# Optimization experiments

Hardware: AMD Instinct MI355X
Metric: run time of the kernel (lower is better)

Reference implementation:

```python
import jax, jax.numpy as jnp
from jax import lax
import numpy as np
import math

D_MODEL = 1024
D_STATE = 16
D_CONV = 4
EXPAND = 2
D_INNER = EXPAND * D_MODEL  # 2048
DT_RANK = math.ceil(D_MODEL / 16)  # 64
BATCH = 2
SEQ = 2048


def setup_inputs() -> dict:
    key = jax.random.key(0)
    ks = jax.random.split(key, 8)
    s = 0.02
    x = jax.random.normal(ks[0], (BATCH, SEQ, D_MODEL), jnp.float32)
    ln_w = jnp.ones((D_MODEL,), jnp.float32)
    ln_b = jnp.zeros((D_MODEL,), jnp.float32)
    in_proj_w = jax.random.normal(ks[1], (D_MODEL, 2 * D_INNER), jnp.float32) * s
    conv_w = jax.random.normal(ks[2], (D_INNER, D_CONV), jnp.float32) * s
    conv_b = jnp.zeros((D_INNER,), jnp.float32)
    x_proj_w = jax.random.normal(ks[3], (D_INNER, DT_RANK + 2 * D_STATE), jnp.float32) * s
    dt_proj_w = jax.random.normal(ks[4], (DT_RANK, D_INNER), jnp.float32) * (DT_RANK ** -0.5)
    # mamba-ssm dt bias init: softplus^{-1}(dt) with dt ~ logUniform(1e-3, 1e-1)
    dt = jnp.exp(jax.random.uniform(ks[5], (D_INNER,), jnp.float32)
                 * (jnp.log(0.1) - jnp.log(0.001)) + jnp.log(0.001))
    dt_proj_b = dt + jnp.log(-jnp.expm1(-dt))
    # S4D-real init: A = -[1..d_state] per channel
    A_log = jnp.log(jnp.broadcast_to(
        jnp.arange(1, D_STATE + 1, dtype=jnp.float32), (D_INNER, D_STATE)))
    D_skip = jnp.ones((D_INNER,), jnp.float32)
    out_proj_w = jax.random.normal(ks[6], (D_INNER, D_MODEL), jnp.float32) * s
    return dict(x=x, ln_w=ln_w, ln_b=ln_b, in_proj_w=in_proj_w, conv_w=conv_w,
                conv_b=conv_b, x_proj_w=x_proj_w, dt_proj_w=dt_proj_w,
                dt_proj_b=dt_proj_b, A_log=A_log, D_skip=D_skip,
                out_proj_w=out_proj_w)


def _layernorm(x, w, b):
    mu = x.mean(-1, keepdims=True)
    var = ((x - mu) ** 2).mean(-1, keepdims=True)
    return (x - mu) * lax.rsqrt(var + 1e-5) * w + b


def _mamba(xn, in_proj_w, conv_w, conv_b, x_proj_w, dt_proj_w, dt_proj_b,
           A_log, D_skip, out_proj_w):
    # in_proj -> split into conv path and gate z
    xz = xn @ in_proj_w                      # [B, L, 2*d_inner]
    xi, z = jnp.split(xz, 2, axis=-1)
    # causal depthwise conv1d over time
    xc = jnp.pad(xi.transpose(0, 2, 1), ((0, 0), (0, 0), (D_CONV - 1, 0)))
    xc = lax.conv_general_dilated(xc, conv_w[:, None, :], (1,), 'VALID',
                                  feature_group_count=D_INNER,
                                  dimension_numbers=('NCH', 'OIH', 'NCH'))
    xc = jax.nn.silu(xc.transpose(0, 2, 1) + conv_b)   # [B, L, d_inner]
    # input-dependent dt, B, C
    dbc = xc @ x_proj_w                      # [B, L, dt_rank + 2*d_state]
    dt = jax.nn.softplus(dbc[..., :DT_RANK] @ dt_proj_w + dt_proj_b)
    Bm = dbc[..., DT_RANK:DT_RANK + D_STATE]  # [B, L, d_state]
    Cm = dbc[..., DT_RANK + D_STATE:]         # [B, L, d_state]
    A = -jnp.exp(A_log)                       # [d_inner, d_state]

    def step(h, inp):
        u_t, dt_t, b_t, c_t = inp             # [B,d_inner],[B,d_inner],[B,S],[B,S]
        h = jnp.exp(dt_t[..., None] * A) * h + (dt_t * u_t)[..., None] * b_t[:, None, :]
        y = jnp.einsum('bds,bs->bd', h, c_t)
        return h, y

    h0 = jnp.zeros((xn.shape[0], D_INNER, D_STATE), xn.dtype)
    _, ys = lax.scan(step, h0, (xc.transpose(1, 0, 2), dt.transpose(1, 0, 2),
                                Bm.transpose(1, 0, 2), Cm.transpose(1, 0, 2)))
    y = ys.transpose(1, 0, 2) + xc * D_skip
    y = y * jax.nn.silu(z)
    return y @ out_proj_w


def reference(x, ln_w, ln_b, in_proj_w, conv_w, conv_b, x_proj_w, dt_proj_w,
              dt_proj_b, A_log, D_skip, out_proj_w):
    xn = _layernorm(x, ln_w, ln_b)
    return x + _mamba(xn, in_proj_w, conv_w, conv_b, x_proj_w, dt_proj_w,
                      dt_proj_b, A_log, D_skip, out_proj_w)
```

## Files before the change

kernel.cpp:

```cpp
#include <hip/hip_runtime.h>
#include <math.h>

#define NROWS 4096
#define DM    1024
#define DI    2048
#define DTR   64
#define DST   16
#define NCHUNK 32
#define CHLEN  64
#define XKS   8
#define XKL   256

typedef __attribute__((ext_vector_type(8))) short bf16x8;
typedef __attribute__((ext_vector_type(4))) float f32x4;

__device__ __forceinline__ unsigned short f2bf(float f) {
  unsigned u = __float_as_uint(f);
  u = (u + 0x7fffu + ((u >> 16) & 1u)) >> 16;
  return (unsigned short)u;
}
__device__ __forceinline__ float softplus_f(float v) {
  return fmaxf(v, 0.f) + log1pf(__expf(-fabsf(v)));
}
__device__ __forceinline__ float silu_f(float v) {
  return v * (1.f / (1.f + __expf(-v)));
}
__device__ __forceinline__ void gload_lds16(const void* g, void* l) {
  __builtin_amdgcn_global_load_lds(
      (const __attribute__((address_space(1))) void*)g,
      (__attribute__((address_space(3))) void*)l, 16, 0, 0);
}

__global__ __launch_bounds__(256) void ln_kernel(const float* __restrict__ x,
                                                 const float* __restrict__ w,
                                                 const float* __restrict__ b,
                                                 unsigned short* __restrict__ xnb) {
  const int row = blockIdx.x;
  const int tid = threadIdx.x;
  const float4 v = ((const float4*)(x + (size_t)row * DM))[tid];
  float s  = v.x + v.y + v.z + v.w;
  float ss = v.x * v.x + v.y * v.y + v.z * v.z + v.w * v.w;
  for (int off = 32; off > 0; off >>= 1) {
    s  += __shfl_down(s, off);
    ss += __shfl_down(ss, off);
  }
  __shared__ float red[4][2];
  if ((tid & 63) == 0) { red[tid >> 6][0] = s; red[tid >> 6][1] = ss; }
  __syncthreads();
  const float fs  = red[0][0] + red[1][0] + red[2][0] + red[3][0];
  const float fss = red[0][1] + red[1][1] + red[2][1] + red[3][1];
  const float mu  = fs * (1.f / DM);
  const float var = fss * (1.f / DM) - mu * mu;
  const float rs  = rsqrtf(var + 1e-5f);
  const float4 wv = ((const float4*)w)[tid];
  const float4 bv = ((const float4*)b)[tid];
  ushort4 o;
  o.x = f2bf((v.x - mu) * rs * wv.x + bv.x);
  o.y = f2bf((v.y - mu) * rs * wv.y + bv.y);
  o.z = f2bf((v.z - mu) * rs * wv.z + bv.z);
  o.w = f2bf((v.w - mu) * rs * wv.w + bv.w);
  ((ushort4*)(xnb + (size_t)row * DM))[tid] = o;
}

__global__ __launch_bounds__(256) void transpose_bf16(const float* __restrict__ W,
                                                      unsigned short* __restrict__ Wt,
                                                      int K, int N) {
  __shared__ float t[32][33];
  const int n0 = blockIdx.x * 32, k0 = blockIdx.y * 32;
  const int tx = threadIdx.x & 31, ty = threadIdx.x >> 5;
#pragma unroll
  for (int i = 0; i < 4; i++)
    t[ty + i * 8][tx] = W[(size_t)(k0 + ty + i * 8) * N + n0 + tx];
  __syncthreads();
#pragma unroll
  for (int i = 0; i < 4; i++)
    Wt[(size_t)(n0 + ty + i * 8) * K + k0 + tx] = f2bf(t[tx][ty + i * 8]);
}

template <int EPI>
__global__ __launch_bounds__(256) void gemm_mfma(
    const unsigned short* __restrict__ A, const unsigned short* __restrict__ Bt,
    float* __restrict__ C, int M, int N, int K, const float* __restrict__ resid) {
  __shared__ unsigned short Asl[128 * 32];
  __shared__ unsigned short Bsl[128 * 32];
  const int tid  = threadIdx.x;
  const int wave = tid >> 6, lane = tid & 63;
  const int wr = wave >> 1, wc = wave & 1;
  const int m0 = blockIdx.y * 128, n0 = blockIdx.x * 128;
  const int srow = lane >> 2;
  const int skoff = (lane & 3) * 8;
  f32x4 acc[4][4] = {};
  for (int k0 = 0; k0 < K; k0 += 32) {
    __syncthreads();
#pragma unroll
    for (int i = 0; i < 2; i++) {
      const int c = wave * 2 + i;
      gload_lds16(A  + (size_t)(m0 + c * 16 + srow) * K + k0 + skoff, &Asl[c * 512]);
      gload_lds16(Bt + (size_t)(n0 + c * 16 + srow) * K + k0 + skoff, &Bsl[c * 512]);
    }
    __syncthreads();
    bf16x8 af[4], bfr[4];
#pragma unroll
    for (int m = 0; m < 4; m++)
      af[m] = *(const bf16x8*)&Asl[(wr * 64 + m * 16 + (lane & 15)) * 32 + (lane >> 4) * 8];
#pragma unroll
    for (int n = 0; n < 4; n++)
      bfr[n] = *(const bf16x8*)&Bsl[(wc * 64 + n * 16 + (lane & 15)) * 32 + (lane >> 4) * 8];
#pragma unroll
    for (int m = 0; m < 4; m++)
#pragma unroll
      for (int n = 0; n < 4; n++)
        acc[m][n] = __builtin_amdgcn_mfma_f32_16x16x32_bf16(af[m], bfr[n], acc[m][n], 0, 0, 0);
  }
#pragma unroll
  for (int m = 0; m < 4; m++) {
#pragma unroll
    for (int n = 0; n < 4; n++) {
      const int col = n0 + wc * 64 + n * 16 + (lane & 15);
#pragma unroll
      for (int r = 0; r < 4; r++) {
        const int row = m0 + wr * 64 + m * 16 + (lane >> 4) * 4 + r;
        float v = acc[m][n][r];
        if (EPI == 2) v += resid[(size_t)row * N + col];
        C[(size_t)row * N + col] = v;
      }
    }
  }
}

__global__ __launch_bounds__(256) void xproj_splitk(
    const float* __restrict__ A,
    const float* __restrict__ B,
    float* __restrict__ part) {
  __shared__ float AsT[32][68];
  __shared__ float Bs[32][96];
  const int ks = blockIdx.x;
  const int r0 = blockIdx.y * 64;
  const int tid = threadIdx.x;
  const int rg = tid >> 4;
  const int cg = tid & 15;
  const int arow = tid >> 2;
  const int ac   = (tid & 3) * 2;
  const int bk   = tid >> 3;
  const int bc   = tid & 7;
  float acc[4][6] = {};
  const int k0base = ks * XKL;
  for (int kt = 0; kt < XKL; kt += 32) {
    const int k0 = k0base + kt;
    const float4 a0 = *(const float4*)&A[(size_t)(r0 + arow) * DI + k0 + ac * 4];
    const float4 a1 = *(const float4*)&A[(size_t)(r0 + arow) * DI + k0 + (ac + 1) * 4];
    const float4 b0 = *(const float4*)&B[(size_t)(k0 + bk) * 96 + bc * 4];
    const float4 b1 = *(const float4*)&B[(size_t)(k0 + bk) * 96 + (bc + 8) * 4];
    const float4 b2 = *(const float4*)&B[(size_t)(k0 + bk) * 96 + (bc + 16) * 4];
    __syncthreads();
#pragma unroll
    for (int j = 0; j < 4; j++) AsT[ac * 4 + j][arow] = (&a0.x)[j];
#pragma unroll
    for (int j = 0; j < 4; j++) AsT[(ac + 1) * 4 + j][arow] = (&a1.x)[j];
    *(float4*)&Bs[bk][bc * 4] = b0;
    *(float4*)&Bs[bk][(bc + 8) * 4] = b1;
    *(float4*)&Bs[bk][(bc + 16) * 4] = b2;
    __syncthreads();
#pragma unroll
    for (int k = 0; k < 32; k++) {
      const float4 av = *(const float4*)&AsT[k][rg * 4];
      const float2 bv0 = *(const float2*)&Bs[k][cg * 6];
      const float2 bv1 = *(const float2*)&Bs[k][cg * 6 + 2];
      const float2 bv2 = *(const float2*)&Bs[k][cg * 6 + 4];
#pragma unroll
      for (int i = 0; i < 4; i++) {
        const float a = (&av.x)[i];
        acc[i][0] += a * bv0.x; acc[i][1] += a * bv0.y;
        acc[i][2] += a * bv1.x; acc[i][3] += a * bv1.y;
        acc[i][4] += a * bv2.x; acc[i][5] += a * bv2.y;
      }
    }
  }
#pragma unroll
  for (int i = 0; i < 4; i++) {
    const int row = r0 + rg * 4 + i;
    float* p = &part[((size_t)ks * NROWS + row) * 96 + cg * 6];
#pragma unroll
    for (int j = 0; j < 3; j++)
      *(float2*)&p[j * 2] = make_float2(acc[i][j * 2], acc[i][j * 2 + 1]);
  }
}

__global__ __launch_bounds__(256) void xproj_reduce(const float* __restrict__ part,
                                                    float* __restrict__ dbc) {
  const int i = blockIdx.x * 256 + threadIdx.x;
  float s = 0.f;
#pragma unroll
  for (int ks = 0; ks < XKS; ks++) s += part[(size_t)ks * (NROWS * 96) + i];
  dbc[i] = s;
}

template <int EPI>
__global__ __launch_bounds__(256) void gemm_kernel(
    const float* __restrict__ A, const float* __restrict__ B,
    float* __restrict__ C, int M, int N, int K, int lda, int ldb, int ldc,
    const float* __restrict__ bias) {
  __shared__ float As[64][20];
  __shared__ float Bs[16][64];
  const int tid = threadIdx.x;
  const int m0 = blockIdx.y * 64, n0 = blockIdx.x * 64;
  const int tx = tid & 15, ty = tid >> 4;
  const int am = tid >> 2, ak4 = (tid & 3) << 2;
  const int bk = tid >> 4, bn4 = (tid & 15) << 2;
  const bool bin = (n0 + bn4) < N;
  float acc[4][4] = {};
  for (int k0 = 0; k0 < K; k0 += 16) {
    const float4 av = *(const float4*)&A[(size_t)(m0 + am) * lda + k0 + ak4];
    float4 bv = make_float4(0.f, 0.f, 0.f, 0.f);
    if (bin) bv = *(const float4*)&B[(size_t)(k0 + bk) * ldb + n0 + bn4];
    __syncthreads();
    *(float4*)&As[am][ak4] = av;
    *(float4*)&Bs[bk][bn4] = bv;
    __syncthreads();
#pragma unroll
    for (int k4 = 0; k4 < 4; k4++) {
      float4 aa[4], bb[4];
#pragma unroll
      for (int i = 0; i < 4; i++) aa[i] = *(const float4*)&As[ty * 4 + i][k4 * 4];
#pragma unroll
      for (int kk = 0; kk < 4; kk++) bb[kk] = *(const float4*)&Bs[k4 * 4 + kk][tx * 4];
#pragma unroll
      for (int kk = 0; kk < 4; kk++) {
#pragma unroll
        for (int i = 0; i < 4; i++) {
          const float a = (&aa[i].x)[kk];
          acc[i][0] += a * bb[kk].x;
          acc[i][1] += a * bb[kk].y;
          acc[i][2] += a * bb[kk].z;
          acc[i][3] += a * bb[kk].w;
        }
      }
    }
  }
#pragma unroll
  for (int i = 0; i < 4; i++) {
    const int row = m0 + ty * 4 + i;
    const int col = n0 + tx * 4;
    if (col < N) {
      float4 o = make_float4(acc[i][0], acc[i][1], acc[i][2], acc[i][3]);
      if (EPI == 1) {
        const float4 bi = *(const float4*)&bias[col];
        o.x = softplus_f(o.x + bi.x);
        o.y = softplus_f(o.y + bi.y);
        o.z = softplus_f(o.z + bi.z);
        o.w = softplus_f(o.w + bi.w);
      }
      *(float4*)&C[(size_t)row * ldc + col] = o;
    }
  }
}

__global__ __launch_bounds__(256) void conv_silu_kernel(const float* __restrict__ xz,
                                                        const float* __restrict__ cw,
                                                        const float* __restrict__ cb,
                                                        float* __restrict__ xc) {
  const int idx = blockIdx.x * 256 + threadIdx.x;
  const int d4 = (idx & 511) << 2;
  const int r = idx >> 9;
  const int t = r & 2047;
  const float4 w0 = *(const float4*)&cw[(d4 + 0) * 4];
  const float4 w1 = *(const float4*)&cw[(d4 + 1) * 4];
  const float4 w2 = *(const float4*)&cw[(d4 + 2) * 4];
  const float4 w3 = *(const float4*)&cw[(d4 + 3) * 4];
  float4 acc = *(const float4*)&cb[d4];
#pragma unroll
  for (int j = 0; j < 4; j++) {
    const int tj = t - 3 + j;
    if (tj >= 0) {
      const float4 xv = *(const float4*)&xz[(size_t)(r - 3 + j) * 4096 + d4];
      acc.x += xv.x * (&w0.x)[j];
      acc.y += xv.y * (&w1.x)[j];
      acc.z += xv.z * (&w2.x)[j];
      acc.w += xv.w * (&w3.x)[j];
    }
  }
  acc.x = silu_f(acc.x); acc.y = silu_f(acc.y);
  acc.z = silu_f(acc.z); acc.w = silu_f(acc.w);
  *(float4*)&xc[(size_t)r * DI + d4] = acc;
}

#define SPF 8
__global__ __launch_bounds__(256) void scan_pass1(
    const float* __restrict__ dt,
    const float* __restrict__ xc,
    const float* __restrict__ dbc,
    const float* __restrict__ A_log,
    float* __restrict__ aprod_buf, float* __restrict__ hout_buf) {
  const int bx = blockIdx.x;
  const int b = bx >> 8, c = (bx >> 3) & 31, dblk = bx & 7;
  const int d = dblk * 256 + threadIdx.x;
  float A2[DST], h[DST], ap[DST];
#pragma unroll
  for (int s = 0; s < DST; s++) {
    A2[s] = -expf(A_log[d * DST + s]) * 1.44269504f;
    h[s] = 0.f; ap[s] = 1.f;
  }
  const int base_r = b * 2048 + c * CHLEN;
  float cdt[SPF], cu[SPF], ndt[SPF], nu[SPF];
#pragma unroll
  for (int j = 0; j < SPF; j++) {
    const size_t r = base_r + j;
    cdt[j] = dt[r * 4096 + d];
    cu[j]  = xc[r * 2048 + d];
  }
  for (int t0 = 0; t0 < CHLEN; t0 += SPF) {
    const bool more = (t0 + SPF) < CHLEN;
    if (more) {
#pragma unroll
      for (int j = 0; j < SPF; j++) {
        const size_t r = base_r + t0 + SPF + j;
        ndt[j] = dt[r * 4096 + d];
        nu[j]  = xc[r * 2048 + d];
      }
    }
#pragma unroll
    for (int j = 0; j < SPF; j++) {
      const float dtv = cdt[j];
      const float du = dtv * cu[j];
      const float* bc = &dbc[(size_t)(base_r + t0 + j) * 96 + DTR];
#pragma unroll
      for (int s = 0; s < DST; s++) {
        const float a = exp2f(dtv * A2[s]);
        h[s] = a * h[s] + du * bc[s];
        ap[s] *= a;
      }
    }
    if (more) {
#pragma unroll
      for (int j = 0; j < SPF; j++) { cdt[j] = ndt[j]; cu[j] = nu[j]; }
    }
  }
  const size_t base = ((size_t)(b * NCHUNK + c) * DST) * DI + d;
#pragma unroll
  for (int s = 0; s < DST; s++) {
    aprod_buf[base + (size_t)s * DI] = ap[s];
    hout_buf[base + (size_t)s * DI]  = h[s];
  }
}

__global__ __launch_bounds__(256) void scan_fixup(const float* __restrict__ aprod_buf,
                                                  float* __restrict__ hout_buf) {
  const int gl = blockIdx.x * 256 + threadIdx.x;
  const int d = gl & 2047, s = (gl >> 11) & 15, b = gl >> 15;
  const size_t base = ((size_t)(b * NCHUNK) * DST + s) * DI + d;
  const size_t stride = (size_t)DST * DI;
  float h = 0.f;
#pragma unroll
  for (int c = 0; c < NCHUNK; c++) {
    const float a = aprod_buf[base + c * stride];
    const float o = hout_buf[base + c * stride];
    hout_buf[base + c * stride] = h;
    h = a * h + o;
  }
}

__global__ __launch_bounds__(256) void scan_pass2(
    const float* __restrict__ dt, const float* __restrict__ xc,
    const float* __restrict__ dbc, const float* __restrict__ A_log,
    const float* __restrict__ Dskip, const float* __restrict__ z,
    const float* __restrict__ hin_buf, unsigned short* __restrict__ y16) {
  const int bx = blockIdx.x;
  const int b = bx >> 8, c = (bx >> 3) & 31, dblk = bx & 7;
  const int d = dblk * 256 + threadIdx.x;
  float A2[DST], h[DST];
  const size_t base = ((size_t)(b * NCHUNK + c) * DST) * DI + d;
#pragma unroll
  for (int s = 0; s < DST; s++) {
    A2[s] = -expf(A_log[d * DST + s]) * 1.44269504f;
    h[s] = hin_buf[base + (size_t)s * DI];
  }
  const float dsk = Dskip[d];
  const int base_r = b * 2048 + c * CHLEN;
  float cdt[SPF], cu[SPF], cz[SPF], ndt[SPF], nu[SPF], nz[SPF];
#pragma unroll
  for (int j = 0; j < SPF; j++) {
    const size_t r = base_r + j;
    cdt[j] = dt[r * 4096 + d];
    cu[j]  = xc[r * 2048 + d];
    cz[j]  = z[r * 4096 + d];
  }
  for (int t0 = 0; t0 < CHLEN; t0 += SPF) {
    const bool more = (t0 + SPF) < CHLEN;
    if (more) {
#pragma unroll
      for (int j = 0; j < SPF; j++) {
        const size_t r = base_r + t0 + SPF + j;
        ndt[j] = dt[r * 4096 + d];
        nu[j]  = xc[r * 2048 + d];
        nz[j]  = z[r * 4096 + d];
      }
    }
#pragma unroll
    for (int j = 0; j < SPF; j++) {
      const size_t r = base_r + t0 + j;
      const float dtv = cdt[j];
      const float uv  = cu[j];
      const float du = dtv * uv;
      const float* bc = &dbc[r * 96 + DTR];
      const float* cc = bc + DST;
      float p0 = 0.f, p1 = 0.f, p2 = 0.f, p3 = 0.f;
#pragma unroll
      for (int s = 0; s < DST; s += 4) {
        float a0 = exp2f(dtv * A2[s + 0]);
        float a1 = exp2f(dtv * A2[s + 1]);
        float a2 = exp2f(dtv * A2[s + 2]);
        float a3 = exp2f(dtv * A2[s + 3]);
        h[s + 0] = a0 * h[s + 0] + du * bc[s + 0];
        h[s + 1] = a1 * h[s + 1] + du * bc[s + 1];
        h[s + 2] = a2 * h[s + 2] + du * bc[s + 2];
        h[s + 3] = a3 * h[s + 3] + du * bc[s + 3];
        p0 += h[s + 0] * cc[s + 0];
        p1 += h[s + 1] * cc[s + 1];
        p2 += h[s + 2] * cc[s + 2];
        p3 += h[s + 3] * cc[s + 3];
      }
      const float y = ((p0 + p1) + (p2 + p3) + uv * dsk) * silu_f(cz[j]);
      y16[r * 2048 + d] = f2bf(y);
    }
    if (more) {
#pragma unroll
      for (int j = 0; j < SPF; j++) { cdt[j] = ndt[j]; cu[j] = nu[j]; cz[j] = nz[j]; }
    }
  }
}

extern "C" void kernel_launch(void* const* d_in, const int* in_sizes, int n_in,
                              void* d_out, int out_size, void* d_ws, size_t ws_size,
                              hipStream_t stream) {
  const float* x         = (const float*)d_in[0];
  const float* ln_w      = (const float*)d_in[1];
  const float* ln_b      = (const float*)d_in[2];
  const float* in_proj_w = (const float*)d_in[3];
  const float* conv_w    = (const float*)d_in[4];
  const float* conv_b    = (const float*)d_in[5];
  const float* x_proj_w  = (const float*)d_in[6];
  const float* dt_proj_w = (const float*)d_in[7];
  const float* dt_proj_b = (const float*)d_in[8];
  const float* A_log     = (const float*)d_in[9];
  const float* D_skip    = (const float*)d_in[10];
  const float* out_proj_w= (const float*)d_in[11];
  float* out = (float*)d_out;
  float* ws  = (float*)d_ws;

  unsigned short* xnb  = (unsigned short*)ws;
  float* part  = ws;
  float* aprod = ws;
  float* hout  = ws + (2u << 20);
  float* xz    = ws + (4u << 20);
  float* xc    = ws + (20u << 20);
  float* dbc   = ws + (28u << 20);
  unsigned short* wtin  = (unsigned short*)(ws + (29u << 20));
  unsigned short* wtout = (unsigned short*)(ws + (31u << 20));
  unsigned short* yb16  = (unsigned short*)(ws + (32u << 20));
  float* dtb = xz;
  float* zp  = xz + DI;

  transpose_bf16<<<dim3(4096 / 32, 1024 / 32), 256, 0, stream>>>(in_proj_w, wtin, DM, 4096);
  transpose_bf16<<<dim3(1024 / 32, 2048 / 32), 256, 0, stream>>>(out_proj_w, wtout, DI, DM);
  ln_kernel<<<NROWS, 256, 0, stream>>>(x, ln_w, ln_b, xnb);
  gemm_mfma<0><<<dim3(32, 32), 256, 0, stream>>>(xnb, wtin, xz, NROWS, 4096, DM, nullptr);
  conv_silu_kernel<<<8192, 256, 0, stream>>>(xz, conv_w, conv_b, xc);
  xproj_splitk<<<dim3(XKS, 64), 256, 0, stream>>>(xc, x_proj_w, part);
  xproj_reduce<<<(NROWS * 96) / 256, 256, 0, stream>>>(part, dbc);
  gemm_kernel<1><<<dim3(32, 64), 256, 0, stream>>>(dbc, dt_proj_w, dtb,
      NROWS, DI, DTR, 96, DI, 4096, dt_proj_b);
  scan_pass1<<<2 * NCHUNK * 8, 256, 0, stream>>>(dtb, xc, dbc, A_log, aprod, hout);
  scan_fixup<<<256, 256, 0, stream>>>(aprod, hout);
  scan_pass2<<<2 * NCHUNK * 8, 256, 0, stream>>>(dtb, xc, dbc, A_log, D_skip, zp, hout, yb16);
  gemm_mfma<2><<<dim3(8, 32), 256, 0, stream>>>(yb16, wtout, out, NROWS, DM, DI, x);
}
```

Measured before the change: 417.2 us.

## Replace chunk decay products with dt sums and double scan chunk count

Pass 1 of the chunked scan now accumulates only the sum of dt per chunk and channel, instead of a running product of exp(dt*A) for every state. The fixup kernel rebuilds each chunk's decay as exp2(A*sum dt). This drops 16 multiplies per timestep and cuts the pass-1 writes roughly in half. The chunk length is also halved (64 chunks of 32 steps), doubling the block count in both scan passes for more parallelism. In exchange the fixup kernel's serial carry chain gets longer and it has more exps to compute.

```diff
diff --git a/kernel.cpp b/kernel.cpp
--- a/kernel.cpp
+++ b/kernel.cpp
@@ -6,8 +6,8 @@
 #define DI    2048
 #define DTR   64
 #define DST   16
-#define NCHUNK 32
-#define CHLEN  64
+#define NCHUNK 64
+#define CHLEN  32
 #define XKS   8
 #define XKL   256
 
@@ -290,16 +290,18 @@
     const float* __restrict__ xc,
     const float* __restrict__ dbc,
     const float* __restrict__ A_log,
-    float* __restrict__ aprod_buf, float* __restrict__ hout_buf) {
+    float* __restrict__ dtsum_buf,
+    float* __restrict__ hout_buf) {
   const int bx = blockIdx.x;
-  const int b = bx >> 8, c = (bx >> 3) & 31, dblk = bx & 7;
+  const int b = bx >> 9, c = (bx >> 3) & 63, dblk = bx & 7;
   const int d = dblk * 256 + threadIdx.x;
-  float A2[DST], h[DST], ap[DST];
+  float A2[DST], h[DST];
 #pragma unroll
   for (int s = 0; s < DST; s++) {
     A2[s] = -expf(A_log[d * DST + s]) * 1.44269504f;
-    h[s] = 0.f; ap[s] = 1.f;
-  }
+    h[s] = 0.f;
+  }
+  float dsum = 0.f;
   const int base_r = b * 2048 + c * CHLEN;
   float cdt[SPF], cu[SPF], ndt[SPF], nu[SPF];
 #pragma unroll
@@ -322,12 +324,12 @@
     for (int j = 0; j < SPF; j++) {
       const float dtv = cdt[j];
       const float du = dtv * cu[j];
+      dsum += dtv;
       const float* bc = &dbc[(size_t)(base_r + t0 + j) * 96 + DTR];
 #pragma unroll
       for (int s = 0; s < DST; s++) {
         const float a = exp2f(dtv * A2[s]);
         h[s] = a * h[s] + du * bc[s];
-        ap[s] *= a;
       }
     }
     if (more) {
@@ -335,26 +337,28 @@
       for (int j = 0; j < SPF; j++) { cdt[j] = ndt[j]; cu[j] = nu[j]; }
     }
   }
+  dtsum_buf[(size_t)(b * NCHUNK + c) * DI + d] = dsum;
   const size_t base = ((size_t)(b * NCHUNK + c) * DST) * DI + d;
 #pragma unroll
-  for (int s = 0; s < DST; s++) {
-    aprod_buf[base + (size_t)s * DI] = ap[s];
-    hout_buf[base + (size_t)s * DI]  = h[s];
-  }
-}
-
-__global__ __launch_bounds__(256) void scan_fixup(const float* __restrict__ aprod_buf,
+  for (int s = 0; s < DST; s++)
+    hout_buf[base + (size_t)s * DI] = h[s];
+}
+
+__global__ __launch_bounds__(256) void scan_fixup(const float* __restrict__ dtsum_buf,
+                                                  const float* __restrict__ A_log,
                                                   float* __restrict__ hout_buf) {
   const int gl = blockIdx.x * 256 + threadIdx.x;
   const int d = gl & 2047, s = (gl >> 11) & 15, b = gl >> 15;
-  const size_t base = ((size_t)(b * NCHUNK) * DST + s) * DI + d;
-  const size_t stride = (size_t)DST * DI;
+  const float A2 = -expf(A_log[d * DST + s]) * 1.44269504f;
+  const size_t hbase = ((size_t)(b * NCHUNK) * DST + s) * DI + d;
+  const size_t hstride = (size_t)DST * DI;
+  const size_t dbase = (size_t)(b * NCHUNK) * DI + d;
   float h = 0.f;
-#pragma unroll
+#pragma unroll 4
   for (int c = 0; c < NCHUNK; c++) {
-    const float a = aprod_buf[base + c * stride];
-    const float o = hout_buf[base + c * stride];
-    hout_buf[base + c * stride] = h;
+    const float a = exp2f(A2 * dtsum_buf[dbase + (size_t)c * DI]);
+    const float o = hout_buf[hbase + c * hstride];
+    hout_buf[hbase + c * hstride] = h;
     h = a * h + o;
   }
 }
@@ -365,7 +369,7 @@
     const float* __restrict__ Dskip, const float* __restrict__ z,
     const float* __restrict__ hin_buf, unsigned short* __restrict__ y16) {
   const int bx = blockIdx.x;
-  const int b = bx >> 8, c = (bx >> 3) & 31, dblk = bx & 7;
+  const int b = bx >> 9, c = (bx >> 3) & 63, dblk = bx & 7;
   const int d = dblk * 256 + threadIdx.x;
   float A2[DST], h[DST];
   const size_t base = ((size_t)(b * NCHUNK + c) * DST) * DI + d;
@@ -449,12 +453,12 @@
 
   unsigned short* xnb  = (unsigned short*)ws;
   float* part  = ws;
-  float* aprod = ws;
-  float* hout  = ws + (2u << 20);
+  float* hout  = ws;
   float* xz    = ws + (4u << 20);
   float* xc    = ws + (20u << 20);
   float* dbc   = ws + (28u << 20);
   unsigned short* wtin  = (unsigned short*)(ws + (29u << 20));
+  float* dtsum = ws + (29u << 20);
   unsigned short* wtout = (unsigned short*)(ws + (31u << 20));
   unsigned short* yb16  = (unsigned short*)(ws + (32u << 20));
   float* dtb = xz;
@@ -469,8 +473,8 @@
   xproj_reduce<<<(NROWS * 96) / 256, 256, 0, stream>>>(part, dbc);
   gemm_kernel<1><<<dim3(32, 64), 256, 0, stream>>>(dbc, dt_proj_w, dtb,
       NROWS, DI, DTR, 96, DI, 4096, dt_proj_b);
-  scan_pass1<<<2 * NCHUNK * 8, 256, 0, stream>>>(dtb, xc, dbc, A_log, aprod, hout);
-  scan_fixup<<<256, 256, 0, stream>>>(aprod, hout);
+  scan_pass1<<<2 * NCHUNK * 8, 256, 0, stream>>>(dtb, xc, dbc, A_log, dtsum, hout);
+  scan_fixup<<<256, 256, 0, stream>>>(dtsum, A_log, hout);
   scan_pass2<<<2 * NCHUNK * 8, 256, 0, stream>>>(dtb, xc, dbc, A_log, D_skip, zp, hout, yb16);
   gemm_mfma<2><<<dim3(8, 32), 256, 0, stream>>>(yb16, wtout, out, NROWS, DM, DI, x);
 }
```

Result: no change. 420.9 us (+0.9%).
